# Performance work log

Measured on AMD Instinct MI355X. Metric: run time of the kernel, lower is better.

## Reference

```python
import jax, jax.numpy as jnp
import numpy as np

B, C, H, W = 8, 32, 256, 256


def setup_inputs() -> dict:
    key = jax.random.key(0)
    k1, k2, k3, k4 = jax.random.split(key, 4)
    shape = (B, C, H, W)
    x = jax.random.normal(k1, shape, dtype=jnp.float32)
    G1 = jax.random.normal(k2, shape, dtype=jnp.float32)
    G2 = jax.random.normal(k3, shape, dtype=jnp.float32)
    G3 = jax.random.normal(k4, shape, dtype=jnp.float32)
    return {"x": x, "G1": G1, "G2": G2, "G3": G3}


def _spn_forward(x, G1, G2, G3):
    # --- SpnBlock gate normalization (elementwise) ---
    sum_abs = jnp.abs(G1) + jnp.abs(G2) + jnp.abs(G3)
    sum_abs = jnp.where(sum_abs == 0, jnp.asarray(1e-6, x.dtype), sum_abs)
    mask = (sum_abs >= 1).astype(x.dtype)  # only normalize where sum(|g|) >= 1
    keep = 1.0 - mask
    G1 = keep * G1 + mask * (G1 / sum_abs)
    G2 = keep * G2 + mask * (G2 / sum_abs)
    G3 = keep * G3 + mask * (G3 / sum_abs)

    # --- GateRecurrent2dnoind (horizontal=True, reverse=False): left->right scan ---
    # h[i,j] = (1 - g1 - g2 - g3) * x[i,j] + g1*h[i-1,j-1] + g2*h[i,j-1] + g3*h[i+1,j-1]
    # Gates whose neighbor is out of range are zeroed (CUDA kernel semantics).
    Hd, Wd = x.shape[2], x.shape[3]
    row = jnp.arange(Hd)
    col_ok = (jnp.arange(Wd) > 0).astype(x.dtype)[None, None, None, :]  # no left col at j=0
    up_ok = (row > 0).astype(x.dtype)[None, None, :, None]
    dn_ok = (row < Hd - 1).astype(x.dtype)[None, None, :, None]
    g1 = G1 * col_ok * up_ok
    g2 = G2 * col_ok
    g3 = G3 * col_ok * dn_ok

    # move scan axis (W) to front: [W, B, C, H]
    xs = jnp.moveaxis(x, 3, 0)
    g1s = jnp.moveaxis(g1, 3, 0)
    g2s = jnp.moveaxis(g2, 3, 0)
    g3s = jnp.moveaxis(g3, 3, 0)

    def step(h_prev, inp):
        xj, a, b, c = inp  # each [B, C, H]
        zero = jnp.zeros_like(h_prev[..., :1])
        up = jnp.concatenate([zero, h_prev[..., :-1]], axis=-1)   # h_prev at row i-1
        dn = jnp.concatenate([h_prev[..., 1:], zero], axis=-1)    # h_prev at row i+1
        h = (1.0 - a - b - c) * xj + a * up + b * h_prev + c * dn
        return h, h

    init = jnp.zeros(x.shape[:3], dtype=x.dtype)  # [B, C, H]
    _, hs = jax.lax.scan(step, init, (xs, g1s, g2s, g3s))
    return jnp.moveaxis(hs, 0, 3)  # back to [B, C, H, W]


def reference(x, G1, G2, G3):
    return _spn_forward(x, G1, G2, G3)
```

## Files before the change

### kernel.cpp

```cpp
#include <hip/hip_runtime.h>


#define HD 256
#define WD 256
#define TW 16
#define NST (WD / TW)

__global__ __launch_bounds__(256) void spn_fwd(
    const float* __restrict__ x, const float* __restrict__ G1,
    const float* __restrict__ G2, const float* __restrict__ G3,
    float* __restrict__ out)
{
    __shared__ float4 sf[TW * HD];
    __shared__ float sh[2][HD + 2];

    const int i = threadIdx.x;
    const size_t base = (size_t)blockIdx.x * (HD * WD) + (size_t)i * WD;
    const float* xr = x  + base;
    const float* ar = G1 + base;
    const float* br = G2 + base;
    const float* cr = G3 + base;
    float* orow = out + base;

    const float upOk = (i > 0) ? 1.f : 0.f;
    const float dnOk = (i < HD - 1) ? 1.f : 0.f;

    float4 px[4], pa[4], pb[4], pc[4];

    {
        const float4* x4 = (const float4*)(xr);
        const float4* a4 = (const float4*)(ar);
        const float4* b4 = (const float4*)(br);
        const float4* c4 = (const float4*)(cr);
#pragma unroll
        for (int k = 0; k < 4; ++k) {
            px[k] = x4[k]; pa[k] = a4[k]; pb[k] = b4[k]; pc[k] = c4[k];
        }
    }

    sh[0][i + 1] = 0.f;
    sh[1][i + 1] = 0.f;
    if (i < 2) { sh[i][0] = 0.f; sh[i][HD + 1] = 0.f; }

    auto stage_write = [&](int j0) {
#pragma unroll
        for (int k = 0; k < 4; ++k) {
            float X[4]  = {px[k].x, px[k].y, px[k].z, px[k].w};
            float A[4]  = {pa[k].x, pa[k].y, pa[k].z, pa[k].w};
            float Bv[4] = {pb[k].x, pb[k].y, pb[k].z, pb[k].w};
            float Cv[4] = {pc[k].x, pc[k].y, pc[k].z, pc[k].w};
#pragma unroll
            for (int e = 0; e < 4; ++e) {
                float a = A[e], b = Bv[e], c = Cv[e];
                float s = fabsf(a) + fabsf(b) + fabsf(c);
                float inv = (s >= 1.f) ? (1.f / s) : 1.f;
                a *= inv; b *= inv; c *= inv;
                float cm = (j0 + k * 4 + e > 0) ? 1.f : 0.f;
                a *= cm * upOk;
                b *= cm;
                c *= cm * dnOk;
                sf[(k * 4 + e) * HD + i] = make_float4(X[e], a, b, c);
            }
        }
    };

    stage_write(0);
    __syncthreads();

    float hprev = 0.f;
#pragma unroll 1
    for (int t = 0; t < NST; ++t) {
        const int j0 = t * TW;

        if (t + 1 < NST) {
            const float4* x4 = (const float4*)(xr + j0 + TW);
            const float4* a4 = (const float4*)(ar + j0 + TW);
            const float4* b4 = (const float4*)(br + j0 + TW);
            const float4* c4 = (const float4*)(cr + j0 + TW);
#pragma unroll
            for (int k = 0; k < 4; ++k) {
                px[k] = x4[k]; pa[k] = a4[k]; pb[k] = b4[k]; pc[k] = c4[k];
            }
        }

        float o[TW];
#pragma unroll
        for (int jj = 0; jj < TW; ++jj) {
            const int rb = jj & 1;
            float4 v = sf[jj * HD + i];
            float up = sh[rb][i];
            float dn = sh[rb][i + 2];
            float h = (1.f - v.y - v.z - v.w) * v.x
                    + v.y * up + v.z * hprev + v.w * dn;
            sh[rb ^ 1][i + 1] = h;
            __syncthreads();
            hprev = h;
            o[jj] = h;
        }

        float4* o4 = (float4*)(orow + j0);
#pragma unroll
        for (int k = 0; k < 4; ++k)
            o4[k] = make_float4(o[4 * k], o[4 * k + 1], o[4 * k + 2], o[4 * k + 3]);

        if (t + 1 < NST) {
            stage_write(j0 + TW);
            __syncthreads();
        }
    }
}

extern "C" void kernel_launch(void* const* d_in, const int* in_sizes, int n_in,
                              void* d_out, int out_size, void* d_ws, size_t ws_size,
                              hipStream_t stream) {
    const float* x  = (const float*)d_in[0];
    const float* g1 = (const float*)d_in[1];
    const float* g2 = (const float*)d_in[2];
    const float* g3 = (const float*)d_in[3];
    float* out = (float*)d_out;
    const int planes = out_size / (HD * WD);
    spn_fwd<<<planes, 256, 0, stream>>>(x, g1, g2, g3, out);
}
```

Before: 104.5 us.

## Rewrite scan as single-wavefront kernel with shuffles and async LDS loads

Each plane is now handled by one 64-lane wavefront, and each lane owns four rows. Vertical neighbour exchange uses wave shuffles instead of shared memory plus __syncthreads on every column, which removes the per-column block barrier. Inputs are double-buffered into LDS with global_load_lds and hand-tuned vmcnt waits. Outputs are transposed through LDS so the global stores coalesce. The cost is a large LDS footprint of one block per CU, with only 256 wavefronts in total and little parallelism to hide latency. The hand-counted waitcnt values are fragile.

```diff
diff --git a/kernel.cpp b/kernel.cpp
--- a/kernel.cpp
+++ b/kernel.cpp
@@ -1,123 +1,136 @@
 #include <hip/hip_runtime.h>
+#include <stdint.h>
 
 
 #define HD 256
 #define WD 256
-#define TW 16
-#define NST (WD / TW)
+#define SW 8
+#define NS (WD / SW)
+#define WIN_B 1040
+#define ARR_B (8 * WIN_B)
+#define STAGE_B (4 * ARR_B)
+#define OUT_STRIDE 260
+#define OUT_OFF (2 * STAGE_B)
 
-__global__ __launch_bounds__(256) void spn_fwd(
+#define F4E(v, e) ((e) == 0 ? (v).x : (e) == 1 ? (v).y : (e) == 2 ? (v).z : (v).w)
+
+__global__ __launch_bounds__(64, 1) void spn_fwd(
     const float* __restrict__ x, const float* __restrict__ G1,
     const float* __restrict__ G2, const float* __restrict__ G3,
     float* __restrict__ out)
 {
-    __shared__ float4 sf[TW * HD];
-    __shared__ float sh[2][HD + 2];
+  __shared__ __align__(16) char lds[83200];
 
-    const int i = threadIdx.x;
-    const size_t base = (size_t)blockIdx.x * (HD * WD) + (size_t)i * WD;
-    const float* xr = x  + base;
-    const float* ar = G1 + base;
-    const float* br = G2 + base;
-    const float* cr = G3 + base;
-    float* orow = out + base;
+  const int l = threadIdx.x;
+  const size_t pbase = (size_t)blockIdx.x * (HD * WD);
+  const float* gp0 = x  + pbase;
+  const float* gp1 = G1 + pbase;
+  const float* gp2 = G2 + pbase;
+  const float* gp3 = G3 + pbase;
+  float* op = out + pbase;
 
-    const float upOk = (i > 0) ? 1.f : 0.f;
-    const float dnOk = (i < HD - 1) ? 1.f : 0.f;
+  const int srow = l >> 1;
+  const int scol = (l & 1) * 4;
 
-    float4 px[4], pa[4], pb[4], pc[4];
+  auto issue_stage = [&](int t, int buf) {
+    char* sb = lds + (buf ? STAGE_B : 0);
+    const int j0 = t * SW;
+    const float* ga_[4] = {gp0, gp1, gp2, gp3};
+#pragma unroll
+    for (int A = 0; A < 4; ++A) {
+      const float* base = ga_[A] + ((size_t)srow * WD + j0 + scol);
+#pragma unroll
+      for (int k = 0; k < 8; ++k) {
+        __builtin_amdgcn_global_load_lds(
+            (const __attribute__((address_space(1))) void*)(base + (size_t)k * 32 * WD),
+            (__attribute__((address_space(3))) void*)(sb + A * ARR_B + k * WIN_B),
+            16, 0, 0);
+      }
+    }
+  };
 
-    {
-        const float4* x4 = (const float4*)(xr);
-        const float4* a4 = (const float4*)(ar);
-        const float4* b4 = (const float4*)(br);
-        const float4* c4 = (const float4*)(cr);
+  const int lb = (l >> 3) * WIN_B + (l & 7) * 128;
+  const float mU = (l > 0) ? 1.f : 0.f;
+  const float mD = (l < 63) ? 1.f : 0.f;
+  float* outldsF = (float*)(lds + OUT_OFF);
+
+  float h[4] = {0.f, 0.f, 0.f, 0.f};
+
+  issue_stage(0, 0);
+  issue_stage(1, 1);
+
+#pragma unroll 1
+  for (int t = 0; t < NS; ++t) {
+    if (t == 0)           asm volatile("s_waitcnt vmcnt(32)" ::: "memory");
+    else if (t == 1)      asm volatile("s_waitcnt vmcnt(40)" ::: "memory");
+    else if (t == NS - 1) asm volatile("s_waitcnt vmcnt(16)" ::: "memory");
+    else                  asm volatile("s_waitcnt vmcnt(48)" ::: "memory");
+
+    const char* sb = lds + ((t & 1) ? STAGE_B : 0);
+    const float cOkF = (t == 0) ? 0.f : 1.f;
+
 #pragma unroll
-        for (int k = 0; k < 4; ++k) {
-            px[k] = x4[k]; pa[k] = a4[k]; pb[k] = b4[k]; pc[k] = c4[k];
+    for (int cc = 0; cc < 2; ++cc) {
+      float4 vx[4], va[4], vb[4], vc[4];
+#pragma unroll
+      for (int r = 0; r < 4; ++r) {
+        const int off = lb + r * 32 + cc * 16;
+        vx[r] = *(const float4*)(sb + 0 * ARR_B + off);
+        va[r] = *(const float4*)(sb + 1 * ARR_B + off);
+        vb[r] = *(const float4*)(sb + 2 * ARR_B + off);
+        vc[r] = *(const float4*)(sb + 3 * ARR_B + off);
+      }
+#pragma unroll
+      for (int e = 0; e < 4; ++e) {
+        const float shU = __shfl_up(h[3], 1);
+        const float shD = __shfl_down(h[0], 1);
+        float hn[4];
+#pragma unroll
+        for (int r = 0; r < 4; ++r) {
+          float aa = F4E(va[r], e), bb = F4E(vb[r], e);
+          float cg = F4E(vc[r], e), xx = F4E(vx[r], e);
+          float s = fabsf(aa) + fabsf(bb) + fabsf(cg);
+          float inv = (s >= 1.f) ? __builtin_amdgcn_rcpf(s) : 1.f;
+          float ga = aa * inv, gb = bb * inv, gc = cg * inv;
+          if (cc == 0 && e == 0) { ga *= cOkF; gb *= cOkF; gc *= cOkF; }
+          if (r == 0) ga *= mU;
+          if (r == 3) gc *= mD;
+          float up = (r == 0) ? shU : h[r - 1];
+          float dn = (r == 3) ? shD : h[r + 1];
+          hn[r] = (1.f - ga - gb - gc) * xx + ga * up + gb * h[r] + gc * dn;
         }
+#pragma unroll
+        for (int r = 0; r < 4; ++r) h[r] = hn[r];
+        *(float4*)(outldsF + (cc * 4 + e) * OUT_STRIDE + 4 * l) =
+            make_float4(hn[0], hn[1], hn[2], hn[3]);
+      }
     }
 
-    sh[0][i + 1] = 0.f;
-    sh[1][i + 1] = 0.f;
-    if (i < 2) { sh[i][0] = 0.f; sh[i][HD + 1] = 0.f; }
+    asm volatile("s_waitcnt lgkmcnt(0)" ::: "memory");
+    if (t + 2 < NS) issue_stage(t + 2, t & 1);
 
-    auto stage_write = [&](int j0) {
+    const int j0 = t * SW;
 #pragma unroll
-        for (int k = 0; k < 4; ++k) {
-            float X[4]  = {px[k].x, px[k].y, px[k].z, px[k].w};
-            float A[4]  = {pa[k].x, pa[k].y, pa[k].z, pa[k].w};
-            float Bv[4] = {pb[k].x, pb[k].y, pb[k].z, pb[k].w};
-            float Cv[4] = {pc[k].x, pc[k].y, pc[k].z, pc[k].w};
-#pragma unroll
-            for (int e = 0; e < 4; ++e) {
-                float a = A[e], b = Bv[e], c = Cv[e];
-                float s = fabsf(a) + fabsf(b) + fabsf(c);
-                float inv = (s >= 1.f) ? (1.f / s) : 1.f;
-                a *= inv; b *= inv; c *= inv;
-                float cm = (j0 + k * 4 + e > 0) ? 1.f : 0.f;
-                a *= cm * upOk;
-                b *= cm;
-                c *= cm * dnOk;
-                sf[(k * 4 + e) * HD + i] = make_float4(X[e], a, b, c);
-            }
-        }
-    };
-
-    stage_write(0);
-    __syncthreads();
-
-    float hprev = 0.f;
-#pragma unroll 1
-    for (int t = 0; t < NST; ++t) {
-        const int j0 = t * TW;
-
-        if (t + 1 < NST) {
-            const float4* x4 = (const float4*)(xr + j0 + TW);
-            const float4* a4 = (const float4*)(ar + j0 + TW);
-            const float4* b4 = (const float4*)(br + j0 + TW);
-            const float4* c4 = (const float4*)(cr + j0 + TW);
-#pragma unroll
-            for (int k = 0; k < 4; ++k) {
-                px[k] = x4[k]; pa[k] = a4[k]; pb[k] = b4[k]; pc[k] = c4[k];
-            }
-        }
-
-        float o[TW];
-#pragma unroll
-        for (int jj = 0; jj < TW; ++jj) {
-            const int rb = jj & 1;
-            float4 v = sf[jj * HD + i];
-            float up = sh[rb][i];
-            float dn = sh[rb][i + 2];
-            float h = (1.f - v.y - v.z - v.w) * v.x
-                    + v.y * up + v.z * hprev + v.w * dn;
-            sh[rb ^ 1][i + 1] = h;
-            __syncthreads();
-            hprev = h;
-            o[jj] = h;
-        }
-
-        float4* o4 = (float4*)(orow + j0);
-#pragma unroll
-        for (int k = 0; k < 4; ++k)
-            o4[k] = make_float4(o[4 * k], o[4 * k + 1], o[4 * k + 2], o[4 * k + 3]);
-
-        if (t + 1 < NST) {
-            stage_write(j0 + TW);
-            __syncthreads();
-        }
+    for (int k = 0; k < 8; ++k) {
+      const int row = k * 32 + srow;
+      float4 o;
+      o.x = outldsF[(scol + 0) * OUT_STRIDE + row];
+      o.y = outldsF[(scol + 1) * OUT_STRIDE + row];
+      o.z = outldsF[(scol + 2) * OUT_STRIDE + row];
+      o.w = outldsF[(scol + 3) * OUT_STRIDE + row];
+      *(float4*)(op + (size_t)row * WD + j0 + scol) = o;
     }
+  }
 }
 
 extern "C" void kernel_launch(void* const* d_in, const int* in_sizes, int n_in,
                               void* d_out, int out_size, void* d_ws, size_t ws_size,
                               hipStream_t stream) {
-    const float* x  = (const float*)d_in[0];
-    const float* g1 = (const float*)d_in[1];
-    const float* g2 = (const float*)d_in[2];
-    const float* g3 = (const float*)d_in[3];
-    float* out = (float*)d_out;
-    const int planes = out_size / (HD * WD);
-    spn_fwd<<<planes, 256, 0, stream>>>(x, g1, g2, g3, out);
+  const float* x  = (const float*)d_in[0];
+  const float* g1 = (const float*)d_in[1];
+  const float* g2 = (const float*)d_in[2];
+  const float* g3 = (const float*)d_in[3];
+  float* outp = (float*)d_out;
+  const int planes = out_size / (HD * WD);
+  spn_fwd<<<planes, 64, 0, stream>>>(x, g1, g2, g3, outp);
 }
```

New measurement: 155.1 us. 1.48x slower.
